# Kernel tuning notes

Hardware: AMD Instinct MI355X
Metric: run time of the kernel (lower is better)

## Reference

```python
import jax, jax.numpy as jnp
import numpy as np

E = 256   # in_features / embed_dim
O = 256   # out_features
H = 8     # n_heads
D = E // H  # head_dim
NEG = -1e9
SLOPE = 0.2  # leaky_relu negative slope


def setup_inputs() -> dict:
    key = jax.random.key(0)
    ks = jax.random.split(key, 9)
    B, N = 8, 1024
    x = jax.random.normal(ks[0], (B, N, E), dtype=jnp.float32)
    adj_matrix = jax.random.randint(ks[1], (N, N), 0, 2, dtype=jnp.int32)
    s = 1.0 / np.sqrt(E)
    w_in = jax.random.uniform(ks[2], (3 * E, E), jnp.float32, -s, s)   # packed q/k/v proj (torch in_proj_weight)
    b_in = jnp.zeros((3 * E,), jnp.float32)
    w_out = jax.random.uniform(ks[3], (E, E), jnp.float32, -s, s)      # MHA out_proj
    b_out = jnp.zeros((E,), jnp.float32)
    w_lin = jax.random.uniform(ks[4], (O, E), jnp.float32, -s, s)      # final nn.Linear
    b_lin = jax.random.uniform(ks[5], (O,), jnp.float32, -s, s)
    return {"x": x, "adj_matrix": adj_matrix, "w_in": w_in, "b_in": b_in,
            "w_out": w_out, "b_out": b_out, "w_lin": w_lin, "b_lin": b_lin}


def reference(x, adj_matrix, w_in, b_in, w_out, b_out, w_lin, b_lin):
    B, N, _ = x.shape
    scale = 1.0 / np.sqrt(D)
    qkv = x @ w_in.T + b_in                      # [B,N,3E]
    q, k, v = jnp.split(qkv, 3, axis=-1)
    q = q.reshape(B, N, H, D) * scale
    k = k.reshape(B, N, H, D)
    v = v.reshape(B, N, H, D)
    scores = jnp.einsum('bnhd,bmhd->bhnm', q, k)  # [B,H,N,N]
    allowed = (adj_matrix != 0)[None, None]       # mask True where adj==0 -> disallowed
    scores = jnp.where(allowed, scores, NEG)
    attn = jax.nn.softmax(scores, axis=-1)
    ctx = jnp.einsum('bhnm,bmhd->bnhd', attn, v).reshape(B, N, E)
    attended = ctx @ w_out.T + b_out              # MHA output (dropout is identity in eval)
    out = attended @ w_lin.T + b_lin
    return jnp.where(out >= 0, out, SLOPE * out)  # leaky_relu(0.2)
```

## Files before the change

### kernel.cpp

```cpp
#include <hip/hip_runtime.h>
#include <math.h>

#define EE 256
#define HH 8
#define DD 32
#define NB 8
#define NS 1024
#define SLOPE 0.2f

typedef float f32x4 __attribute__((ext_vector_type(4)));
typedef short short8 __attribute__((ext_vector_type(8)));

static __device__ __forceinline__ unsigned short f2b(float f) {
    unsigned int u = __float_as_uint(f);
    u = (u + 0x7FFFu + ((u >> 16) & 1u)) >> 16;
    return (unsigned short)u;
}

static __device__ __forceinline__ unsigned int cvtpk(float lo, float hi) {
    unsigned int r;
    asm("v_cvt_pk_bf16_f32 %0, %1, %2" : "=v"(r) : "v"(lo), "v"(hi));
    return r;
}

static __device__ __forceinline__ void gload_lds16(const void* g, void* l) {
    __builtin_amdgcn_global_load_lds(
        (const __attribute__((address_space(1))) unsigned int*)g,
        (__attribute__((address_space(3))) unsigned int*)l, 16, 0, 0);
}

__global__ __launch_bounds__(256) void prep(
    const float* __restrict__ x, const float* __restrict__ wi,
    const float* __restrict__ wo, const float* __restrict__ bo,
    const float* __restrict__ wl, const float* __restrict__ bl,
    const int* __restrict__ adj,
    unsigned short* __restrict__ xb, unsigned short* __restrict__ wib,
    unsigned short* __restrict__ wcb, float* __restrict__ bcomb,
    unsigned int* __restrict__ bits) {
    int blk = blockIdx.x;
    if (blk < 1120) {
        int t = blk * 256 + threadIdx.x;
        const float* src; unsigned short* dst; int base;
        if (t < 262144) { src = x;  dst = xb;  base = t; }
        else            { src = wi; dst = wib; base = t - 262144; }
        const float4* s = (const float4*)(src + (size_t)base * 8);
        float4 a = s[0], b = s[1];
        uint4 wv;
        wv.x = cvtpk(a.x, a.y); wv.y = cvtpk(a.z, a.w);
        wv.z = cvtpk(b.x, b.y); wv.w = cvtpk(b.z, b.w);
        *(uint4*)(dst + (size_t)base * 8) = wv;
    } else if (blk < 1248) {
        int t = (blk - 1120) * 256 + threadIdx.x;
        int n = t >> 5, w = t & 31;
        const int* p = adj + (size_t)n * NS + w * 32;
        unsigned int word = 0;
#pragma unroll
        for (int i = 0; i < 32; i += 4) {
            int4 a = *(const int4*)(p + i);
            if (a.x) word |= 1u << i;
            if (a.y) word |= 1u << (i + 1);
            if (a.z) word |= 1u << (i + 2);
            if (a.w) word |= 1u << (i + 3);
        }
        bits[t] = word;
    } else {
        int o = blk - 1248, c = threadIdx.x;
        const float* wlr = wl + (size_t)o * EE;
        float acc = 0.f;
#pragma unroll 8
        for (int e = 0; e < EE; ++e)
            acc = fmaf(wlr[e], wo[(size_t)e * EE + c], acc);
        wcb[(size_t)o * EE + c] = f2b(acc);
        if (c == 0) {
            float bb = bl[o];
            for (int e = 0; e < EE; ++e) bb = fmaf(wlr[e], bo[e], bb);
            bcomb[o] = bb;
        }
    }
}

template<int MODE>
__global__ __launch_bounds__(256) void gemm_mfma(
    const unsigned short* __restrict__ A, const unsigned short* __restrict__ W,
    const float* __restrict__ bias, void* __restrict__ out,
    unsigned short* __restrict__ qb, unsigned short* __restrict__ kb,
    unsigned short* __restrict__ vtb, int Nout) {
    __shared__ __align__(16) unsigned short As[128 * 64];
    __shared__ __align__(16) unsigned short Bs[64 * 64];
    int tid = threadIdx.x, w = tid >> 6, lane = tid & 63;
    int lq = lane & 15, g = lane >> 4;
    int wr = w >> 1, wc = w & 1;
    int m0 = blockIdx.y * 128, n0 = blockIdx.x * 64;
    int r8 = lane >> 3, c8 = (lane & 7) * 8;
    f32x4 acc[4][2];
#pragma unroll
    for (int i = 0; i < 4; ++i)
#pragma unroll
        for (int j = 0; j < 2; ++j) acc[i][j] = (f32x4){0.f, 0.f, 0.f, 0.f};

    for (int k0 = 0; k0 < 256; k0 += 64) {
        __syncthreads();
#pragma unroll
        for (int i = 0; i < 4; ++i)
            gload_lds16(A + (size_t)(m0 + w * 32 + i * 8 + r8) * 256 + k0 + c8,
                        &As[(w * 32 + i * 8) * 64]);
#pragma unroll
        for (int i = 0; i < 2; ++i)
            gload_lds16(W + (size_t)(n0 + w * 16 + i * 8 + r8) * 256 + k0 + c8,
                        &Bs[(w * 16 + i * 8) * 64]);
        __syncthreads();
#pragma unroll
        for (int ks = 0; ks < 2; ++ks) {
            short8 af[4], bf[2];
#pragma unroll
            for (int mi = 0; mi < 4; ++mi)
                af[mi] = *(const short8*)(&As[(wr * 64 + mi * 16 + lq) * 64 + ks * 32 + g * 8]);
#pragma unroll
            for (int ni = 0; ni < 2; ++ni)
                bf[ni] = *(const short8*)(&Bs[(wc * 32 + ni * 16 + lq) * 64 + ks * 32 + g * 8]);
#pragma unroll
            for (int mi = 0; mi < 4; ++mi)
#pragma unroll
                for (int ni = 0; ni < 2; ++ni)
                    acc[mi][ni] = __builtin_amdgcn_mfma_f32_16x16x32_bf16(af[mi], bf[ni], acc[mi][ni], 0, 0, 0);
        }
    }
    const float scale = 0.17677669529663687f;
#pragma unroll
    for (int mi = 0; mi < 4; ++mi) {
#pragma unroll
        for (int reg = 0; reg < 4; ++reg) {
            int m = m0 + wr * 64 + mi * 16 + g * 4 + reg;
#pragma unroll
            for (int ni = 0; ni < 2; ++ni) {
                int n = n0 + wc * 32 + ni * 16 + lq;
                float v = acc[mi][ni][reg] + bias[n];
                if (MODE == 1) {
                    v = v >= 0.f ? v : SLOPE * v;
                    ((float*)out)[(size_t)m * Nout + n] = v;
                } else {
                    int sec = n >> 8, cc = n & 255, h = cc >> 5, d = cc & 31;
                    int b = m >> 10, nr = m & (NS - 1);
                    if (sec == 0)
                        qb[((size_t)(b * HH + h) * NS + nr) * DD + d] = f2b(v * scale);
                    else if (sec == 1)
                        kb[((size_t)(b * HH + h) * NS + nr) * DD + d] = f2b(v);
                    else {
                        int nrp = (nr & ~31) | ((nr & 12) << 1) | ((nr & 16) >> 2) | (nr & 3);
                        vtb[((size_t)(b * HH + h) * DD + d) * NS + nrp] = f2b(v);
                    }
                }
            }
        }
    }
}

__global__ __launch_bounds__(256) void attn_mfma(
    const unsigned short* __restrict__ q, const unsigned short* __restrict__ k,
    const unsigned short* __restrict__ vt, const unsigned int* __restrict__ adjbits,
    unsigned short* __restrict__ ctx) {
    __shared__ __align__(16) unsigned short Ks[2][128 * 40];
    __shared__ __align__(16) unsigned short Vs[2][32 * 136];
    int tid = threadIdx.x;
    int w = tid >> 6, lane = tid & 63;
    int lq = lane & 15, g = lane >> 4;
    int bh = blockIdx.y;
    int n0 = blockIdx.x * 64;
    int nq = n0 + w * 16 + lq;
    const unsigned short* qb = q + (size_t)bh * NS * DD;
    const unsigned short* kbp = k + (size_t)bh * NS * DD;
    const unsigned short* vbp = vt + (size_t)bh * DD * NS;
    short8 qfrag = *(const short8*)(qb + (size_t)nq * DD + g * 8);
    const unsigned int* abr = adjbits + (size_t)nq * 32;
    float lsA = 0.f, lsB = 0.f;
    f32x4 acc0 = {0.f, 0.f, 0.f, 0.f}, acc1 = {0.f, 0.f, 0.f, 0.f};
    int kr = tid >> 1, kc = (tid & 1) * 16;
    int vd = tid >> 3, vc = (tid & 7) * 16;
    const unsigned short* kst = kbp + (size_t)kr * DD + kc;
    const unsigned short* vst = vbp + (size_t)vd * NS + vc;

    int4 ka = *(const int4*)(kst);
    int4 kb2 = *(const int4*)(kst + 8);
    int4 va = *(const int4*)(vst);
    int4 vb2 = *(const int4*)(vst + 8);
    *(int4*)(&Ks[0][kr * 40 + kc])     = ka;
    *(int4*)(&Ks[0][kr * 40 + kc + 8]) = kb2;
    *(int4*)(&Vs[0][vd * 136 + vc])     = va;
    *(int4*)(&Vs[0][vd * 136 + vc + 8]) = vb2;
    __syncthreads();

    int c = 0;
    for (int t = 0; t < 8; ++t) {
        if (t < 7) {
            const unsigned short* kn = kst + (size_t)(t + 1) * 128 * DD;
            const unsigned short* vn = vst + (size_t)(t + 1) * 128;
            ka  = *(const int4*)(kn);
            kb2 = *(const int4*)(kn + 8);
            va  = *(const int4*)(vn);
            vb2 = *(const int4*)(vn + 8);
        }
        const unsigned short* ksl = Ks[c];
        const unsigned short* vsl = Vs[c];
        uint4 w4 = *(const uint4*)(abr + t * 4);
        const f32x4 z = {0.f, 0.f, 0.f, 0.f};
        __builtin_amdgcn_s_setprio(1);
#pragma unroll
        for (int T = 0; T < 4; ++T) {
            unsigned int wdT = (T == 0) ? w4.x : (T == 1) ? w4.y : (T == 2) ? w4.z : w4.w;
            short8 kf0 = *(const short8*)(&ksl[(32 * T + lq) * 40 + g * 8]);
            short8 kf1 = *(const short8*)(&ksl[(32 * T + 16 + lq) * 40 + g * 8]);
            f32x4 s0 = __builtin_amdgcn_mfma_f32_16x16x32_bf16(kf0, qfrag, z, 0, 0, 0);
            f32x4 s1 = __builtin_amdgcn_mfma_f32_16x16x32_bf16(kf1, qfrag, z, 0, 0, 0);
            unsigned int b0 = wdT >> (4 * g);
            unsigned int b1 = wdT >> (16 + 4 * g);
            float p0 = ((b0 >> 0) & 1u) ? __expf(s0[0]) : 0.f;
            float p1 = ((b0 >> 1) & 1u) ? __expf(s0[1]) : 0.f;
            float p2 = ((b0 >> 2) & 1u) ? __expf(s0[2]) : 0.f;
            float p3 = ((b0 >> 3) & 1u) ? __expf(s0[3]) : 0.f;
            float p4 = ((b1 >> 0) & 1u) ? __expf(s1[0]) : 0.f;
            float p5 = ((b1 >> 1) & 1u) ? __expf(s1[1]) : 0.f;
            float p6 = ((b1 >> 2) & 1u) ? __expf(s1[2]) : 0.f;
            float p7 = ((b1 >> 3) & 1u) ? __expf(s1[3]) : 0.f;
            lsA += (p0 + p1) + (p2 + p3);
            lsB += (p4 + p5) + (p6 + p7);
            union { uint4 u; short8 s; } pb;
            pb.u.x = cvtpk(p0, p1); pb.u.y = cvtpk(p2, p3);
            pb.u.z = cvtpk(p4, p5); pb.u.w = cvtpk(p6, p7);
            short8 va0 = *(const short8*)(&vsl[lq * 136 + T * 32 + g * 8]);
            short8 va1 = *(const short8*)(&vsl[(16 + lq) * 136 + T * 32 + g * 8]);
            acc0 = __builtin_amdgcn_mfma_f32_16x16x32_bf16(va0, pb.s, acc0, 0, 0, 0);
            acc1 = __builtin_amdgcn_mfma_f32_16x16x32_bf16(va1, pb.s, acc1, 0, 0, 0);
        }
        __builtin_amdgcn_s_setprio(0);
        if (t < 7) {
            *(int4*)(&Ks[c ^ 1][kr * 40 + kc])     = ka;
            *(int4*)(&Ks[c ^ 1][kr * 40 + kc + 8]) = kb2;
            *(int4*)(&Vs[c ^ 1][vd * 136 + vc])     = va;
            *(int4*)(&Vs[c ^ 1][vd * 136 + vc + 8]) = vb2;
        }
        __syncthreads();
        c ^= 1;
    }
    float rs = lsA + lsB;
    rs += __shfl_xor(rs, 16);
    rs += __shfl_xor(rs, 32);
    float inv = 1.f / rs;
    int b = bh >> 3, h = bh & 7;
    unsigned short* dst = ctx + ((size_t)(b * NS + nq)) * EE + h * DD;
    uint2 o0, o1;
    o0.x = cvtpk(acc0[0] * inv, acc0[1] * inv);
    o0.y = cvtpk(acc0[2] * inv, acc0[3] * inv);
    o1.x = cvtpk(acc1[0] * inv, acc1[1] * inv);
    o1.y = cvtpk(acc1[2] * inv, acc1[3] * inv);
    *(uint2*)(dst + 4 * g) = o0;
    *(uint2*)(dst + 16 + 4 * g) = o1;
}

extern "C" void kernel_launch(void* const* d_in, const int* in_sizes, int n_in,
                              void* d_out, int out_size, void* d_ws, size_t ws_size,
                              hipStream_t stream) {
    const float* x     = (const float*)d_in[0];
    const int*   adj   = (const int*)d_in[1];
    const float* w_in  = (const float*)d_in[2];
    const float* b_in  = (const float*)d_in[3];
    const float* w_out = (const float*)d_in[4];
    const float* b_out = (const float*)d_in[5];
    const float* w_lin = (const float*)d_in[6];
    const float* b_lin = (const float*)d_in[7];
    float* out = (float*)d_out;

    const size_t S = (size_t)NB * HH * NS * DD;
    unsigned short* qb   = (unsigned short*)d_ws;
    unsigned short* kb   = qb + S;
    unsigned short* vtb  = kb + S;
    unsigned short* ctxb = vtb + S;
    unsigned short* xb   = ctxb + S;
    unsigned short* wib  = xb + S;
    unsigned short* wcb  = wib + 768 * 256;
    unsigned int* adjbits = (unsigned int*)(wcb + 256 * 256);
    float* bcomb = (float*)(adjbits + 32768);

    dim3 blk(256);
    prep<<<dim3(1504), blk, 0, stream>>>(x, w_in, w_out, b_out, w_lin, b_lin, adj,
                                         xb, wib, wcb, bcomb, adjbits);
    gemm_mfma<2><<<dim3(12, 64), blk, 0, stream>>>(xb, wib, b_in, nullptr, qb, kb, vtb, 768);
    attn_mfma<<<dim3(NS / 64, NB * HH), blk, 0, stream>>>(qb, kb, vtb, adjbits, ctxb);
    gemm_mfma<1><<<dim3(4, 64), blk, 0, stream>>>(ctxb, wcb, bcomb, out, nullptr, nullptr, nullptr, 256);
}
```

Baseline: 72.34 us.

## Fuse all four stages into one persistent cooperative kernel with grid syncs

Replaces the four separate launches (prep, QKV GEMM, attention, output GEMM) with a single cooperative persistent kernel. Blocks loop over virtual block indices and stages are separated by grid-wide syncs, with GEMM and attention shared memory overlaid in a union. The goal is to remove launch gaps and per-kernel tail effects. In exchange it adds grid-sync cost, caps concurrency at the occupancy-derived block count, and may lose the per-kernel register and occupancy tuning the separate kernels had.

```diff
diff --git a/kernel.cpp b/kernel.cpp
--- a/kernel.cpp
+++ b/kernel.cpp
@@ -1,5 +1,8 @@
 #include <hip/hip_runtime.h>
+#include <hip/hip_cooperative_groups.h>
 #include <math.h>
+
+namespace cg = cooperative_groups;
 
 #define EE 256
 #define HH 8
@@ -29,68 +32,32 @@
         (__attribute__((address_space(3))) unsigned int*)l, 16, 0, 0);
 }
 
-__global__ __launch_bounds__(256) void prep(
-    const float* __restrict__ x, const float* __restrict__ wi,
-    const float* __restrict__ wo, const float* __restrict__ bo,
-    const float* __restrict__ wl, const float* __restrict__ bl,
-    const int* __restrict__ adj,
-    unsigned short* __restrict__ xb, unsigned short* __restrict__ wib,
-    unsigned short* __restrict__ wcb, float* __restrict__ bcomb,
-    unsigned int* __restrict__ bits) {
-    int blk = blockIdx.x;
-    if (blk < 1120) {
-        int t = blk * 256 + threadIdx.x;
-        const float* src; unsigned short* dst; int base;
-        if (t < 262144) { src = x;  dst = xb;  base = t; }
-        else            { src = wi; dst = wib; base = t - 262144; }
-        const float4* s = (const float4*)(src + (size_t)base * 8);
-        float4 a = s[0], b = s[1];
-        uint4 wv;
-        wv.x = cvtpk(a.x, a.y); wv.y = cvtpk(a.z, a.w);
-        wv.z = cvtpk(b.x, b.y); wv.w = cvtpk(b.z, b.w);
-        *(uint4*)(dst + (size_t)base * 8) = wv;
-    } else if (blk < 1248) {
-        int t = (blk - 1120) * 256 + threadIdx.x;
-        int n = t >> 5, w = t & 31;
-        const int* p = adj + (size_t)n * NS + w * 32;
-        unsigned int word = 0;
-#pragma unroll
-        for (int i = 0; i < 32; i += 4) {
-            int4 a = *(const int4*)(p + i);
-            if (a.x) word |= 1u << i;
-            if (a.y) word |= 1u << (i + 1);
-            if (a.z) word |= 1u << (i + 2);
-            if (a.w) word |= 1u << (i + 3);
-        }
-        bits[t] = word;
-    } else {
-        int o = blk - 1248, c = threadIdx.x;
-        const float* wlr = wl + (size_t)o * EE;
-        float acc = 0.f;
-#pragma unroll 8
-        for (int e = 0; e < EE; ++e)
-            acc = fmaf(wlr[e], wo[(size_t)e * EE + c], acc);
-        wcb[(size_t)o * EE + c] = f2b(acc);
-        if (c == 0) {
-            float bb = bl[o];
-            for (int e = 0; e < EE; ++e) bb = fmaf(wlr[e], bo[e], bb);
-            bcomb[o] = bb;
-        }
-    }
-}
+struct Params {
+    const float* x; const int* adj;
+    const float* w_in; const float* b_in;
+    const float* w_out; const float* b_out;
+    const float* w_lin; const float* b_lin;
+    float* out;
+    unsigned short *qb, *kb, *vtb, *ctxb, *xb, *wib, *wcb;
+    unsigned int* adjbits; float* bcomb;
+    int nb;
+};
+
+union __align__(16) SharedU {
+    struct { unsigned short As[128 * 64]; unsigned short Bs[64 * 64]; } g;
+    struct { unsigned short Ks[2][128 * 40]; unsigned short Vs[2][32 * 136]; } a;
+};
 
 template<int MODE>
-__global__ __launch_bounds__(256) void gemm_mfma(
+static __device__ __forceinline__ void gemm_tile(
+    unsigned short* As, unsigned short* Bs, int tid,
     const unsigned short* __restrict__ A, const unsigned short* __restrict__ W,
     const float* __restrict__ bias, void* __restrict__ out,
     unsigned short* __restrict__ qb, unsigned short* __restrict__ kb,
-    unsigned short* __restrict__ vtb, int Nout) {
-    __shared__ __align__(16) unsigned short As[128 * 64];
-    __shared__ __align__(16) unsigned short Bs[64 * 64];
-    int tid = threadIdx.x, w = tid >> 6, lane = tid & 63;
+    unsigned short* __restrict__ vtb, int Nout, int m0, int n0) {
+    int w = tid >> 6, lane = tid & 63;
     int lq = lane & 15, g = lane >> 4;
     int wr = w >> 1, wc = w & 1;
-    int m0 = blockIdx.y * 128, n0 = blockIdx.x * 64;
     int r8 = lane >> 3, c8 = (lane & 7) * 8;
     f32x4 acc[4][2];
 #pragma unroll
@@ -155,120 +122,164 @@
     }
 }
 
-__global__ __launch_bounds__(256) void attn_mfma(
-    const unsigned short* __restrict__ q, const unsigned short* __restrict__ k,
-    const unsigned short* __restrict__ vt, const unsigned int* __restrict__ adjbits,
-    unsigned short* __restrict__ ctx) {
-    __shared__ __align__(16) unsigned short Ks[2][128 * 40];
-    __shared__ __align__(16) unsigned short Vs[2][32 * 136];
-    int tid = threadIdx.x;
-    int w = tid >> 6, lane = tid & 63;
-    int lq = lane & 15, g = lane >> 4;
-    int bh = blockIdx.y;
-    int n0 = blockIdx.x * 64;
-    int nq = n0 + w * 16 + lq;
-    const unsigned short* qb = q + (size_t)bh * NS * DD;
-    const unsigned short* kbp = k + (size_t)bh * NS * DD;
-    const unsigned short* vbp = vt + (size_t)bh * DD * NS;
-    short8 qfrag = *(const short8*)(qb + (size_t)nq * DD + g * 8);
-    const unsigned int* abr = adjbits + (size_t)nq * 32;
-    float lsA = 0.f, lsB = 0.f;
-    f32x4 acc0 = {0.f, 0.f, 0.f, 0.f}, acc1 = {0.f, 0.f, 0.f, 0.f};
-    int kr = tid >> 1, kc = (tid & 1) * 16;
-    int vd = tid >> 3, vc = (tid & 7) * 16;
-    const unsigned short* kst = kbp + (size_t)kr * DD + kc;
-    const unsigned short* vst = vbp + (size_t)vd * NS + vc;
-
-    int4 ka = *(const int4*)(kst);
-    int4 kb2 = *(const int4*)(kst + 8);
-    int4 va = *(const int4*)(vst);
-    int4 vb2 = *(const int4*)(vst + 8);
-    *(int4*)(&Ks[0][kr * 40 + kc])     = ka;
-    *(int4*)(&Ks[0][kr * 40 + kc + 8]) = kb2;
-    *(int4*)(&Vs[0][vd * 136 + vc])     = va;
-    *(int4*)(&Vs[0][vd * 136 + vc + 8]) = vb2;
-    __syncthreads();
-
-    int c = 0;
-    for (int t = 0; t < 8; ++t) {
-        if (t < 7) {
-            const unsigned short* kn = kst + (size_t)(t + 1) * 128 * DD;
-            const unsigned short* vn = vst + (size_t)(t + 1) * 128;
-            ka  = *(const int4*)(kn);
-            kb2 = *(const int4*)(kn + 8);
-            va  = *(const int4*)(vn);
-            vb2 = *(const int4*)(vn + 8);
+__global__ __launch_bounds__(256, 4) void fused(Params p) {
+    __shared__ SharedU sh;
+    cg::grid_group gg = cg::this_grid();
+    const int tid = threadIdx.x;
+    const int nb = p.nb;
+
+    for (int vb = blockIdx.x; vb < 1504; vb += nb) {
+        if (vb < 1120) {
+            int t = vb * 256 + tid;
+            const float* src; unsigned short* dst; int base;
+            if (t < 262144) { src = p.x;    dst = p.xb;  base = t; }
+            else            { src = p.w_in; dst = p.wib; base = t - 262144; }
+            const float4* s = (const float4*)(src + (size_t)base * 8);
+            float4 a = s[0], b = s[1];
+            uint4 wv;
+            wv.x = cvtpk(a.x, a.y); wv.y = cvtpk(a.z, a.w);
+            wv.z = cvtpk(b.x, b.y); wv.w = cvtpk(b.z, b.w);
+            *(uint4*)(dst + (size_t)base * 8) = wv;
+        } else if (vb < 1248) {
+            int t = (vb - 1120) * 256 + tid;
+            int n = t >> 5, w = t & 31;
+            const int* pp = p.adj + (size_t)n * NS + w * 32;
+            unsigned int word = 0;
+#pragma unroll
+            for (int i = 0; i < 32; i += 4) {
+                int4 a = *(const int4*)(pp + i);
+                if (a.x) word |= 1u << i;
+                if (a.y) word |= 1u << (i + 1);
+                if (a.z) word |= 1u << (i + 2);
+                if (a.w) word |= 1u << (i + 3);
+            }
+            p.adjbits[t] = word;
+        } else {
+            int o = vb - 1248, c = tid;
+            const float* wlr = p.w_lin + (size_t)o * EE;
+            float acc = 0.f;
+#pragma unroll 8
+            for (int e = 0; e < EE; ++e)
+                acc = fmaf(wlr[e], p.w_out[(size_t)e * EE + c], acc);
+            p.wcb[(size_t)o * EE + c] = f2b(acc);
+            if (c == 0) {
+                float bb = p.b_lin[o];
+                for (int e = 0; e < EE; ++e) bb = fmaf(wlr[e], p.b_out[e], bb);
+                p.bcomb[o] = bb;
+            }
         }
-        const unsigned short* ksl = Ks[c];
-        const unsigned short* vsl = Vs[c];
-        uint4 w4 = *(const uint4*)(abr + t * 4);
-        const f32x4 z = {0.f, 0.f, 0.f, 0.f};
-        __builtin_amdgcn_s_setprio(1);
-#pragma unroll
-        for (int T = 0; T < 4; ++T) {
-            unsigned int wdT = (T == 0) ? w4.x : (T == 1) ? w4.y : (T == 2) ? w4.z : w4.w;
-            short8 kf0 = *(const short8*)(&ksl[(32 * T + lq) * 40 + g * 8]);
-            short8 kf1 = *(const short8*)(&ksl[(32 * T + 16 + lq) * 40 + g * 8]);
-            f32x4 s0 = __builtin_amdgcn_mfma_f32_16x16x32_bf16(kf0, qfrag, z, 0, 0, 0);
-            f32x4 s1 = __builtin_amdgcn_mfma_f32_16x16x32_bf16(kf1, qfrag, z, 0, 0, 0);
-            unsigned int b0 = wdT >> (4 * g);
-            unsigned int b1 = wdT >> (16 + 4 * g);
-            float p0 = ((b0 >> 0) & 1u) ? __expf(s0[0]) : 0.f;
-            float p1 = ((b0 >> 1) & 1u) ? __expf(s0[1]) : 0.f;
-            float p2 = ((b0 >> 2) & 1u) ? __expf(s0[2]) : 0.f;
-            float p3 = ((b0 >> 3) & 1u) ? __expf(s0[3]) : 0.f;
-            float p4 = ((b1 >> 0) & 1u) ? __expf(s1[0]) : 0.f;
-            float p5 = ((b1 >> 1) & 1u) ? __expf(s1[1]) : 0.f;
-            float p6 = ((b1 >> 2) & 1u) ? __expf(s1[2]) : 0.f;
-            float p7 = ((b1 >> 3) & 1u) ? __expf(s1[3]) : 0.f;
-            lsA += (p0 + p1) + (p2 + p3);
-            lsB += (p4 + p5) + (p6 + p7);
-            union { uint4 u; short8 s; } pb;
-            pb.u.x = cvtpk(p0, p1); pb.u.y = cvtpk(p2, p3);
-            pb.u.z = cvtpk(p4, p5); pb.u.w = cvtpk(p6, p7);
-            short8 va0 = *(const short8*)(&vsl[lq * 136 + T * 32 + g * 8]);
-            short8 va1 = *(const short8*)(&vsl[(16 + lq) * 136 + T * 32 + g * 8]);
-            acc0 = __builtin_amdgcn_mfma_f32_16x16x32_bf16(va0, pb.s, acc0, 0, 0, 0);
-            acc1 = __builtin_amdgcn_mfma_f32_16x16x32_bf16(va1, pb.s, acc1, 0, 0, 0);
+    }
+    gg.sync();
+
+    for (int vb = blockIdx.x; vb < 768; vb += nb)
+        gemm_tile<2>(sh.g.As, sh.g.Bs, tid, p.xb, p.wib, p.b_in, nullptr,
+                     p.qb, p.kb, p.vtb, 768, (vb / 12) * 128, (vb % 12) * 64);
+    gg.sync();
+
+    for (int vb = blockIdx.x; vb < 1024; vb += nb) {
+        int bh = vb >> 4;
+        int n0 = (vb & 15) * 64;
+        int w = tid >> 6, lane = tid & 63;
+        int lq = lane & 15, g = lane >> 4;
+        int nq = n0 + w * 16 + lq;
+        const unsigned short* qbp = p.qb + (size_t)bh * NS * DD;
+        const unsigned short* kbp = p.kb + (size_t)bh * NS * DD;
+        const unsigned short* vbp = p.vtb + (size_t)bh * DD * NS;
+        short8 qfrag = *(const short8*)(qbp + (size_t)nq * DD + g * 8);
+        const unsigned int* abr = p.adjbits + (size_t)nq * 32;
+        float lsA = 0.f, lsB = 0.f;
+        f32x4 acc0 = {0.f, 0.f, 0.f, 0.f}, acc1 = {0.f, 0.f, 0.f, 0.f};
+        int kr = tid >> 1, kc = (tid & 1) * 16;
+        int vd = tid >> 3, vc = (tid & 7) * 16;
+        const unsigned short* kst = kbp + (size_t)kr * DD + kc;
+        const unsigned short* vst = vbp + (size_t)vd * NS + vc;
+
+        int4 ka = *(const int4*)(kst);
+        int4 kb2 = *(const int4*)(kst + 8);
+        int4 va = *(const int4*)(vst);
+        int4 vb2 = *(const int4*)(vst + 8);
+        *(int4*)(&sh.a.Ks[0][kr * 40 + kc])     = ka;
+        *(int4*)(&sh.a.Ks[0][kr * 40 + kc + 8]) = kb2;
+        *(int4*)(&sh.a.Vs[0][vd * 136 + vc])     = va;
+        *(int4*)(&sh.a.Vs[0][vd * 136 + vc + 8]) = vb2;
+        __syncthreads();
+
+        int c = 0;
+        for (int t = 0; t < 8; ++t) {
+            if (t < 7) {
+                const unsigned short* kn = kst + (size_t)(t + 1) * 128 * DD;
+                const unsigned short* vn = vst + (size_t)(t + 1) * 128;
+                ka  = *(const int4*)(kn);
+                kb2 = *(const int4*)(kn + 8);
+                va  = *(const int4*)(vn);
+                vb2 = *(const int4*)(vn + 8);
+            }
+            const unsigned short* ksl = sh.a.Ks[c];
+            const unsigned short* vsl = sh.a.Vs[c];
+            uint4 w4 = *(const uint4*)(abr + t * 4);
+            const f32x4 z = {0.f, 0.f, 0.f, 0.f};
+            __builtin_amdgcn_s_setprio(1);
+#pragma unroll
+            for (int T = 0; T < 4; ++T) {
+                unsigned int wdT = (T == 0) ? w4.x : (T == 1) ? w4.y : (T == 2) ? w4.z : w4.w;
+                short8 kf0 = *(const short8*)(&ksl[(32 * T + lq) * 40 + g * 8]);
+                short8 kf1 = *(const short8*)(&ksl[(32 * T + 16 + lq) * 40 + g * 8]);
+                f32x4 s0 = __builtin_amdgcn_mfma_f32_16x16x32_bf16(kf0, qfrag, z, 0, 0, 0);
+                f32x4 s1 = __builtin_amdgcn_mfma_f32_16x16x32_bf16(kf1, qfrag, z, 0, 0, 0);
+                unsigned int b0 = wdT >> (4 * g);
+                unsigned int b1 = wdT >> (16 + 4 * g);
+                float p0 = ((b0 >> 0) & 1u) ? __expf(s0[0]) : 0.f;
+                float p1 = ((b0 >> 1) & 1u) ? __expf(s0[1]) : 0.f;
+                float p2 = ((b0 >> 2) & 1u) ? __expf(s0[2]) : 0.f;
+                float p3 = ((b0 >> 3) & 1u) ? __expf(s0[3]) : 0.f;
+                float p4 = ((b1 >> 0) & 1u) ? __expf(s1[0]) : 0.f;
+                float p5 = ((b1 >> 1) & 1u) ? __expf(s1[1]) : 0.f;
+                float p6 = ((b1 >> 2) & 1u) ? __expf(s1[2]) : 0.f;
+                float p7 = ((b1 >> 3) & 1u) ? __expf(s1[3]) : 0.f;
+                lsA += (p0 + p1) + (p2 + p3);
+                lsB += (p4 + p5) + (p6 + p7);
+                union { uint4 u; short8 s; } pb;
+                pb.u.x = cvtpk(p0, p1); pb.u.y = cvtpk(p2, p3);
+                pb.u.z = cvtpk(p4, p5); pb.u.w = cvtpk(p6, p7);
+                short8 va0 = *(const short8*)(&vsl[lq * 136 + T * 32 + g * 8]);
+                short8 va1 = *(const short8*)(&vsl[(16 + lq) * 136 + T * 32 + g * 8]);
+                acc0 = __builtin_amdgcn_mfma_f32_16x16x32_bf16(va0, pb.s, acc0, 0, 0, 0);
+                acc1 = __builtin_amdgcn_mfma_f32_16x16x32_bf16(va1, pb.s, acc1, 0, 0, 0);
+            }
+            __builtin_amdgcn_s_setprio(0);
+            if (t < 7) {
+                *(int4*)(&sh.a.Ks[c ^ 1][kr * 40 + kc])     = ka;
+                *(int4*)(&sh.a.Ks[c ^ 1][kr * 40 + kc + 8]) = kb2;
+                *(int4*)(&sh.a.Vs[c ^ 1][vd * 136 + vc])     = va;
+                *(int4*)(&sh.a.Vs[c ^ 1][vd * 136 + vc + 8]) = vb2;
+            }
+            __syncthreads();
+            c ^= 1;
         }
-        __builtin_amdgcn_s_setprio(0);
-        if (t < 7) {
-            *(int4*)(&Ks[c ^ 1][kr * 40 + kc])     = ka;
-            *(int4*)(&Ks[c ^ 1][kr * 40 + kc + 8]) = kb2;
-            *(int4*)(&Vs[c ^ 1][vd * 136 + vc])     = va;
-            *(int4*)(&Vs[c ^ 1][vd * 136 + vc + 8]) = vb2;
-        }
-        __syncthreads();
-        c ^= 1;
+        float rs = lsA + lsB;
+        rs += __shfl_xor(rs, 16);
+        rs += __shfl_xor(rs, 32);
+        float inv = 1.f / rs;
+        int b = bh >> 3, h = bh & 7;
+        unsigned short* dst = p.ctxb + ((size_t)(b * NS + nq)) * EE + h * DD;
+        uint2 o0, o1;
+        o0.x = cvtpk(acc0[0] * inv, acc0[1] * inv);
+        o0.y = cvtpk(acc0[2] * inv, acc0[3] * inv);
+        o1.x = cvtpk(acc1[0] * inv, acc1[1] * inv);
+        o1.y = cvtpk(acc1[2] * inv, acc1[3] * inv);
+        *(uint2*)(dst + 4 * g) = o0;
+        *(uint2*)(dst + 16 + 4 * g) = o1;
     }
-    float rs = lsA + lsB;
-    rs += __shfl_xor(rs, 16);
-    rs += __shfl_xor(rs, 32);
-    float inv = 1.f / rs;
-    int b = bh >> 3, h = bh & 7;
-    unsigned short* dst = ctx + ((size_t)(b * NS + nq)) * EE + h * DD;
-    uint2 o0, o1;
-    o0.x = cvtpk(acc0[0] * inv, acc0[1] * inv);
-    o0.y = cvtpk(acc0[2] * inv, acc0[3] * inv);
-    o1.x = cvtpk(acc1[0] * inv, acc1[1] * inv);
-    o1.y = cvtpk(acc1[2] * inv, acc1[3] * inv);
-    *(uint2*)(dst + 4 * g) = o0;
-    *(uint2*)(dst + 16 + 4 * g) = o1;
+    gg.sync();
+
+    for (int vb = blockIdx.x; vb < 256; vb += nb)
+        gemm_tile<1>(sh.g.As, sh.g.Bs, tid, p.ctxb, p.wcb, p.bcomb, p.out,
+                     nullptr, nullptr, nullptr, 256, (vb / 4) * 128, (vb % 4) * 64);
 }
 
 extern "C" void kernel_launch(void* const* d_in, const int* in_sizes, int n_in,
                               void* d_out, int out_size, void* d_ws, size_t ws_size,
                               hipStream_t stream) {
-    const float* x     = (const float*)d_in[0];
-    const int*   adj   = (const int*)d_in[1];
-    const float* w_in  = (const float*)d_in[2];
-    const float* b_in  = (const float*)d_in[3];
-    const float* w_out = (const float*)d_in[4];
-    const float* b_out = (const float*)d_in[5];
-    const float* w_lin = (const float*)d_in[6];
-    const float* b_lin = (const float*)d_in[7];
-    float* out = (float*)d_out;
-
     const size_t S = (size_t)NB * HH * NS * DD;
     unsigned short* qb   = (unsigned short*)d_ws;
     unsigned short* kb   = qb + S;
@@ -280,10 +291,27 @@
     unsigned int* adjbits = (unsigned int*)(wcb + 256 * 256);
     float* bcomb = (float*)(adjbits + 32768);
 
-    dim3 blk(256);
-    prep<<<dim3(1504), blk, 0, stream>>>(x, w_in, w_out, b_out, w_lin, b_lin, adj,
-                                         xb, wib, wcb, bcomb, adjbits);
-    gemm_mfma<2><<<dim3(12, 64), blk, 0, stream>>>(xb, wib, b_in, nullptr, qb, kb, vtb, 768);
-    attn_mfma<<<dim3(NS / 64, NB * HH), blk, 0, stream>>>(qb, kb, vtb, adjbits, ctxb);
-    gemm_mfma<1><<<dim3(4, 64), blk, 0, stream>>>(ctxb, wcb, bcomb, out, nullptr, nullptr, nullptr, 256);
-}
+    Params p;
+    p.x     = (const float*)d_in[0];
+    p.adj   = (const int*)d_in[1];
+    p.w_in  = (const float*)d_in[2];
+    p.b_in  = (const float*)d_in[3];
+    p.w_out = (const float*)d_in[4];
+    p.b_out = (const float*)d_in[5];
+    p.w_lin = (const float*)d_in[6];
+    p.b_lin = (const float*)d_in[7];
+    p.out   = (float*)d_out;
+    p.qb = qb; p.kb = kb; p.vtb = vtb; p.ctxb = ctxb;
+    p.xb = xb; p.wib = wib; p.wcb = wcb;
+    p.adjbits = adjbits; p.bcomb = bcomb;
+
+    int bpc = 0;
+    if (hipOccupancyMaxActiveBlocksPerMultiprocessor(&bpc, (const void*)fused, 256, 0) != hipSuccess || bpc <= 0)
+        bpc = 4;
+    int nb = 256 * bpc;
+    if (nb > 1024) nb = 1024;
+    p.nb = nb;
+
+    void* args[] = { &p };
+    hipLaunchCooperativeKernel((const void*)fused, dim3(nb), dim3(256), args, 0, stream);
+}
```

New measurement: 267.4 us. +269.6%, slower.

## Remap block indices for XCD locality and halve output GEMM tile height

Applied to the files above, without the earlier changes.

Flattens the grids and remaps block IDs so consecutive blocks dispatched to the same XCD (round-robin over 8) share the same A rows or batch-head, improving L2 reuse of K/V and activations. The output projection GEMM now uses 64-row tiles, doubling its block count from 256 to 512 so more CUs are occupied. The trade-off is smaller per-block reuse in that GEMM and mapping logic that assumes 8 XCDs.

```diff
diff --git a/kernel.cpp b/kernel.cpp
--- a/kernel.cpp
+++ b/kernel.cpp
@@ -79,31 +79,42 @@
     }
 }
 
-template<int MODE>
+template<int MODE, int BM>
 __global__ __launch_bounds__(256) void gemm_mfma(
     const unsigned short* __restrict__ A, const unsigned short* __restrict__ W,
     const float* __restrict__ bias, void* __restrict__ out,
     unsigned short* __restrict__ qb, unsigned short* __restrict__ kb,
     unsigned short* __restrict__ vtb, int Nout) {
-    __shared__ __align__(16) unsigned short As[128 * 64];
+    const int MI = BM / 32;
+    __shared__ __align__(16) unsigned short As[BM * 64];
     __shared__ __align__(16) unsigned short Bs[64 * 64];
     int tid = threadIdx.x, w = tid >> 6, lane = tid & 63;
     int lq = lane & 15, g = lane >> 4;
     int wr = w >> 1, wc = w & 1;
-    int m0 = blockIdx.y * 128, n0 = blockIdx.x * 64;
+    int f = blockIdx.x;
+    int m0, n0;
+    if (MODE == 2) {
+        int xcd = f & 7, i = f >> 3;
+        m0 = (xcd * 8 + i / 12) * 128;
+        n0 = (i % 12) * 64;
+    } else {
+        int xcd = f & 7, i = f >> 3;
+        m0 = (xcd * 16 + (i >> 2)) * 64;
+        n0 = (i & 3) * 64;
+    }
     int r8 = lane >> 3, c8 = (lane & 7) * 8;
-    f32x4 acc[4][2];
-#pragma unroll
-    for (int i = 0; i < 4; ++i)
+    f32x4 acc[MI][2];
+#pragma unroll
+    for (int i = 0; i < MI; ++i)
 #pragma unroll
         for (int j = 0; j < 2; ++j) acc[i][j] = (f32x4){0.f, 0.f, 0.f, 0.f};
 
     for (int k0 = 0; k0 < 256; k0 += 64) {
         __syncthreads();
 #pragma unroll
-        for (int i = 0; i < 4; ++i)
-            gload_lds16(A + (size_t)(m0 + w * 32 + i * 8 + r8) * 256 + k0 + c8,
-                        &As[(w * 32 + i * 8) * 64]);
+        for (int i = 0; i < MI; ++i)
+            gload_lds16(A + (size_t)(m0 + w * (BM / 4) + i * 8 + r8) * 256 + k0 + c8,
+                        &As[(w * (BM / 4) + i * 8) * 64]);
 #pragma unroll
         for (int i = 0; i < 2; ++i)
             gload_lds16(W + (size_t)(n0 + w * 16 + i * 8 + r8) * 256 + k0 + c8,
@@ -111,15 +122,15 @@
         __syncthreads();
 #pragma unroll
         for (int ks = 0; ks < 2; ++ks) {
-            short8 af[4], bf[2];
-#pragma unroll
-            for (int mi = 0; mi < 4; ++mi)
-                af[mi] = *(const short8*)(&As[(wr * 64 + mi * 16 + lq) * 64 + ks * 32 + g * 8]);
+            short8 af[MI], bf[2];
+#pragma unroll
+            for (int mi = 0; mi < MI; ++mi)
+                af[mi] = *(const short8*)(&As[(wr * (BM / 2) + mi * 16 + lq) * 64 + ks * 32 + g * 8]);
 #pragma unroll
             for (int ni = 0; ni < 2; ++ni)
                 bf[ni] = *(const short8*)(&Bs[(wc * 32 + ni * 16 + lq) * 64 + ks * 32 + g * 8]);
 #pragma unroll
-            for (int mi = 0; mi < 4; ++mi)
+            for (int mi = 0; mi < MI; ++mi)
 #pragma unroll
                 for (int ni = 0; ni < 2; ++ni)
                     acc[mi][ni] = __builtin_amdgcn_mfma_f32_16x16x32_bf16(af[mi], bf[ni], acc[mi][ni], 0, 0, 0);
@@ -127,10 +138,10 @@
     }
     const float scale = 0.17677669529663687f;
 #pragma unroll
-    for (int mi = 0; mi < 4; ++mi) {
+    for (int mi = 0; mi < MI; ++mi) {
 #pragma unroll
         for (int reg = 0; reg < 4; ++reg) {
-            int m = m0 + wr * 64 + mi * 16 + g * 4 + reg;
+            int m = m0 + wr * (BM / 2) + mi * 16 + g * 4 + reg;
 #pragma unroll
             for (int ni = 0; ni < 2; ++ni) {
                 int n = n0 + wc * 32 + ni * 16 + lq;
@@ -164,8 +175,10 @@
     int tid = threadIdx.x;
     int w = tid >> 6, lane = tid & 63;
     int lq = lane & 15, g = lane >> 4;
-    int bh = blockIdx.y;
-    int n0 = blockIdx.x * 64;
+    int f = blockIdx.x;
+    int xcd = f & 7, i = f >> 3;
+    int bh = xcd * 8 + (i >> 4);
+    int n0 = (i & 15) * 64;
     int nq = n0 + w * 16 + lq;
     const unsigned short* qb = q + (size_t)bh * NS * DD;
     const unsigned short* kbp = k + (size_t)bh * NS * DD;
@@ -283,7 +296,7 @@
     dim3 blk(256);
     prep<<<dim3(1504), blk, 0, stream>>>(x, w_in, w_out, b_out, w_lin, b_lin, adj,
                                          xb, wib, wcb, bcomb, adjbits);
-    gemm_mfma<2><<<dim3(12, 64), blk, 0, stream>>>(xb, wib, b_in, nullptr, qb, kb, vtb, 768);
-    attn_mfma<<<dim3(NS / 64, NB * HH), blk, 0, stream>>>(qb, kb, vtb, adjbits, ctxb);
-    gemm_mfma<1><<<dim3(4, 64), blk, 0, stream>>>(ctxb, wcb, bcomb, out, nullptr, nullptr, nullptr, 256);
-}
+    gemm_mfma<2, 128><<<dim3(768), blk, 0, stream>>>(xb, wib, b_in, nullptr, qb, kb, vtb, 768);
+    attn_mfma<<<dim3(1024), blk, 0, stream>>>(qb, kb, vtb, adjbits, ctxb);
+    gemm_mfma<1, 64><<<dim3(512), blk, 0, stream>>>(ctxb, wcb, bcomb, out, nullptr, nullptr, nullptr, 256);
+}
```

Result: faster. 67.52 us (-6.7%).
